# Kernel optimization log

Measured on AMD Instinct MI355X. Metric: run time of the kernel, lower is better.

Reference implementation:

```python
import jax, jax.numpy as jnp
import numpy as np


def setup_inputs() -> dict:
    key = jax.random.key(0)
    k1, k2, k3, k4, k5 = jax.random.split(key, 5)
    b, c, k, h, w = 8, 512, 19, 128, 128
    x = jax.random.normal(k1, (b, c, h, w), dtype=jnp.float32)
    # mask_conv: 1x1 conv ichn->ochn (weight [k, c], bias [k])
    Wm = jax.random.normal(k2, (k, c), dtype=jnp.float32) * (1.0 / np.sqrt(c))
    bm = jax.random.normal(k3, (k,), dtype=jnp.float32) * 0.02
    # filter_conv: grouped 1x1 conv, groups=k -> per-class [c_out, c_in] matmul
    Wf = jax.random.normal(k4, (k, c, c), dtype=jnp.float32) * (1.0 / np.sqrt(c))
    bf = jax.random.normal(k5, (k, c), dtype=jnp.float32) * 0.02
    return {"x": x, "Wm": Wm, "bm": bm, "Wf": Wf, "bf": bf}


def reference(x, Wm, bm, Wf, bf):
    b, c, h, w = x.shape
    k = Wm.shape[0]
    # mask_conv (1x1) + sigmoid -> [b, k, h, w]
    pre_mask = jnp.einsum('bchw,kc->bkhw', x, Wm) + bm[None, :, None, None]
    mask = jax.nn.sigmoid(pre_mask)
    # masked pooling: bmm(mask [b,k,hw], feat [b,hw,c]) / (h*w) -> [b, k, c]
    class_feat = jnp.einsum('bkhw,bchw->bkc', mask, x) / (h * w)
    # grouped 1x1 filter_conv: per class k, [c_out, c_in] GEMM on class_feat
    filters = jnp.einsum('koc,bkc->bko', Wf, class_feat) + bf[None, :, :]  # [b, k, c]
    # per-sample dynamic 1x1 conv (groups=b) == batched GEMM over channels
    pred = jnp.einsum('bkc,bchw->bkhw', filters, x)
    return pred
```

## Files before the change

kernel.cpp:

```cpp
#include <hip/hip_runtime.h>
#include <math.h>

#define BB 8
#define CC 512
#define KK 19
#define HWHW 16384
#define INV_HW (1.0f/16384.0f)

typedef __attribute__((ext_vector_type(8))) short bf16x8;
typedef __attribute__((ext_vector_type(4))) short s16x4;
typedef __attribute__((ext_vector_type(4))) float f32x4;

__device__ __forceinline__ unsigned short f2bf(float f) {
    unsigned int u = __float_as_uint(f);
    u = (u + 0x7fffu + ((u >> 16) & 1u)) >> 16;
    return (unsigned short)u;
}

__global__ __launch_bounds__(256) void k_s1(const float* __restrict__ x,
                                            const float* __restrict__ Wm,
                                            const float* __restrict__ bm,
                                            unsigned short* __restrict__ mask) {
    __shared__ short wm[20 * CC];
    __shared__ short xt[128 * 64];
    const int tid = threadIdx.x;
    const int b = blockIdx.x >> 7;
    const int p0 = (blockIdx.x & 127) << 7;
    const float* xb = x + ((size_t)b * CC) * HWHW + p0;

    for (int u = tid; u < 20 * 128; u += 256) {
        const int k = u >> 7;
        const int c4 = (u & 127) << 2;
        float4 w = {0.f, 0.f, 0.f, 0.f};
        if (k < KK) w = *(const float4*)(Wm + k * CC + c4);
        s16x4 v = { (short)f2bf(w.x), (short)f2bf(w.y), (short)f2bf(w.z), (short)f2bf(w.w) };
        *(s16x4*)&wm[(k << 9) + (((c4 >> 3) ^ (k & 7)) << 3) + (c4 & 7)] = v;
    }

    const int wv = tid >> 6, ln = tid & 63;
    const int lm = ln & 15, q = ln >> 4;
    const f32x4 zz = {0.f, 0.f, 0.f, 0.f};
    f32x4 acc[2][2];
    acc[0][0] = zz; acc[0][1] = zz; acc[1][0] = zz; acc[1][1] = zz;

    for (int cs = 0; cs < 8; ++cs) {
        __syncthreads();
#pragma unroll
        for (int r = 0; r < 2; ++r) {
            const int u = tid + (r << 8);
            const int cg = u >> 5;
            const int p = (u & 31) << 2;
            const float* src = xb + (size_t)((cs << 6) + (cg << 2)) * HWHW + p;
            float4 F0 = *(const float4*)(src);
            float4 F1 = *(const float4*)(src + HWHW);
            float4 F2 = *(const float4*)(src + 2 * HWHW);
            float4 F3 = *(const float4*)(src + 3 * HWHW);
            const float* G0 = (const float*)&F0;
            const float* G1 = (const float*)&F1;
            const float* G2 = (const float*)&F2;
            const float* G3 = (const float*)&F3;
#pragma unroll
            for (int j = 0; j < 4; ++j) {
                const int pr = p + j;
                s16x4 v = { (short)f2bf(G0[j]), (short)f2bf(G1[j]),
                            (short)f2bf(G2[j]), (short)f2bf(G3[j]) };
                *(s16x4*)&xt[(pr << 6) + (((cg >> 1) ^ (pr & 7)) << 3) + ((cg & 1) << 2)] = v;
            }
        }
        __syncthreads();
#pragma unroll
        for (int ks = 0; ks < 2; ++ks) {
            const int gch = (cs << 3) + (ks << 2) + q;
            const int m1 = (lm < 3) ? (16 + lm) : 19;
            bf16x8 a0 = *(const bf16x8*)&wm[(lm << 9) + ((gch ^ (lm & 7)) << 3)];
            bf16x8 a1 = *(const bf16x8*)&wm[(m1 << 9) + ((gch ^ (m1 & 7)) << 3)];
            const int lch = (ks << 2) + q;
#pragma unroll
            for (int nt = 0; nt < 2; ++nt) {
                const int pr = (((wv << 1) + nt) << 4) + lm;
                bf16x8 bf_ = *(const bf16x8*)&xt[(pr << 6) + ((lch ^ (pr & 7)) << 3)];
                acc[0][nt] = __builtin_amdgcn_mfma_f32_16x16x32_bf16(a0, bf_, acc[0][nt], 0, 0, 0);
                acc[1][nt] = __builtin_amdgcn_mfma_f32_16x16x32_bf16(a1, bf_, acc[1][nt], 0, 0, 0);
            }
        }
    }

    unsigned short* mb = mask + ((size_t)b * KK) * HWHW + p0;
#pragma unroll
    for (int mt = 0; mt < 2; ++mt)
#pragma unroll
        for (int r = 0; r < 4; ++r) {
            const int k = (mt << 4) + (q << 2) + r;
            if (k < KK) {
                const float bias = bm[k];
#pragma unroll
                for (int nt = 0; nt < 2; ++nt) {
                    const int p = (((wv << 1) + nt) << 4) + lm;
                    const float t = acc[mt][nt][r] + bias;
                    mb[(size_t)k * HWHW + p] = f2bf(1.0f / (1.0f + __expf(-t)));
                }
            }
        }
}

__global__ __launch_bounds__(256) void k_s2(const float* __restrict__ x,
                                            const unsigned short* __restrict__ mask,
                                            float* __restrict__ cf_part) {
    __shared__ short mt_[20 * 64];
    __shared__ short xtl[64 * 64];
    const int tid = threadIdx.x;
    const int s = blockIdx.x & 15;
    const int ct = (blockIdx.x >> 4) & 7;
    const int b = blockIdx.x >> 7;
    const int wv = tid >> 6, ln = tid & 63;
    const int lm = ln & 15, q = ln >> 4;
    const float* xb = x + ((size_t)b * CC + (ct << 6)) * HWHW + (s << 10);
    const unsigned short* mbs = mask + ((size_t)b * KK) * HWHW + (s << 10);

    const f32x4 zz = {0.f, 0.f, 0.f, 0.f};
    f32x4 acc[2];
    acc[0] = zz; acc[1] = zz;

    for (int kp = 0; kp < 16; ++kp) {
        __syncthreads();
        if (tid < 160) {
            const int k = tid >> 3, ch = tid & 7;
            uint4 v = {0u, 0u, 0u, 0u};
            if (k < KK) v = *(const uint4*)(mbs + (size_t)k * HWHW + (kp << 6) + (ch << 3));
            *(uint4*)&mt_[(k << 6) + ((ch ^ (k & 7)) << 3)] = v;
        }
#pragma unroll
        for (int r = 0; r < 4; ++r) {
            const int u = tid + (r << 8);
            const int c = u >> 4;
            const int pq = u & 15;
            float4 f = *(const float4*)(xb + (size_t)c * HWHW + (kp << 6) + (pq << 2));
            s16x4 v = { (short)f2bf(f.x), (short)f2bf(f.y), (short)f2bf(f.z), (short)f2bf(f.w) };
            *(s16x4*)&xtl[(c << 6) + (((pq >> 1) ^ (c & 7)) << 3) + ((pq & 1) << 2)] = v;
        }
        __syncthreads();
#pragma unroll
        for (int ks = 0; ks < 2; ++ks) {
            const int pch = (ks << 2) + q;
            const int cr = (wv << 4) + lm;
            bf16x8 bf_ = *(const bf16x8*)&xtl[(cr << 6) + ((pch ^ (cr & 7)) << 3)];
            const int m1 = (lm < 3) ? (16 + lm) : 19;
            bf16x8 a0 = *(const bf16x8*)&mt_[(lm << 6) + ((pch ^ (lm & 7)) << 3)];
            bf16x8 a1 = *(const bf16x8*)&mt_[(m1 << 6) + ((pch ^ (m1 & 7)) << 3)];
            acc[0] = __builtin_amdgcn_mfma_f32_16x16x32_bf16(a0, bf_, acc[0], 0, 0, 0);
            acc[1] = __builtin_amdgcn_mfma_f32_16x16x32_bf16(a1, bf_, acc[1], 0, 0, 0);
        }
    }

    float* dst = cf_part + ((size_t)(s * BB + b) * KK) * CC + (ct << 6) + (wv << 4) + lm;
#pragma unroll
    for (int mt = 0; mt < 2; ++mt)
#pragma unroll
        for (int r = 0; r < 4; ++r) {
            const int k = (mt << 4) + (q << 2) + r;
            if (k < KK) dst[(size_t)k * CC] = acc[mt][r];
        }
}

__global__ __launch_bounds__(256) void k_s2r(const float* __restrict__ part,
                                             float* __restrict__ cf) {
    const int i = blockIdx.x * 256 + threadIdx.x;
    if (i >= BB * KK * CC) return;
    const int b = i / (KK * CC);
    const int rem = i - b * (KK * CC);
    float sum = 0.0f;
#pragma unroll
    for (int s = 0; s < 16; ++s)
        sum += part[((size_t)(s * BB + b) * KK) * CC + rem];
    cf[i] = sum * INV_HW;
}

__global__ __launch_bounds__(256) void k_filters(const float* __restrict__ Wf,
                                                 const float* __restrict__ bf,
                                                 const float* __restrict__ cf,
                                                 float* __restrict__ fil) {
    const int blk = blockIdx.x;
    const int k = blk >> 7;
    const int o = ((blk & 127) << 2) + (threadIdx.x >> 6);
    const int lane = threadIdx.x & 63;
    const float* wrow = Wf + ((size_t)k * CC + o) * CC;

    float acc[BB];
#pragma unroll
    for (int b = 0; b < BB; ++b) acc[b] = 0.0f;
#pragma unroll
    for (int j = 0; j < CC / 64; ++j) {
        const int c = lane + (j << 6);
        const float wv = wrow[c];
#pragma unroll
        for (int b = 0; b < BB; ++b)
            acc[b] += wv * cf[((size_t)b * KK + k) * CC + c];
    }
#pragma unroll
    for (int b = 0; b < BB; ++b) {
#pragma unroll
        for (int off = 32; off > 0; off >>= 1)
            acc[b] += __shfl_down(acc[b], off, 64);
    }
    if (lane == 0) {
        const float bias = bf[k * CC + o];
#pragma unroll
        for (int b = 0; b < BB; ++b)
            fil[((size_t)b * KK + k) * CC + o] = acc[b] + bias;
    }
}

__global__ __launch_bounds__(256) void k_s4(const float* __restrict__ x,
                                            const float* __restrict__ fil,
                                            float* __restrict__ out) {
    __shared__ short wm[20 * CC];
    __shared__ short xt[128 * 64];
    const int tid = threadIdx.x;
    const int b = blockIdx.x >> 7;
    const int p0 = (blockIdx.x & 127) << 7;
    const float* xb = x + ((size_t)b * CC) * HWHW + p0;
    const float* fb = fil + ((size_t)b * KK) * CC;

    for (int u = tid; u < 20 * 128; u += 256) {
        const int k = u >> 7;
        const int c4 = (u & 127) << 2;
        float4 w = {0.f, 0.f, 0.f, 0.f};
        if (k < KK) w = *(const float4*)(fb + k * CC + c4);
        s16x4 v = { (short)f2bf(w.x), (short)f2bf(w.y), (short)f2bf(w.z), (short)f2bf(w.w) };
        *(s16x4*)&wm[(k << 9) + (((c4 >> 3) ^ (k & 7)) << 3) + (c4 & 7)] = v;
    }

    const int wv = tid >> 6, ln = tid & 63;
    const int lm = ln & 15, q = ln >> 4;
    const f32x4 zz = {0.f, 0.f, 0.f, 0.f};
    f32x4 acc[2][2];
    acc[0][0] = zz; acc[0][1] = zz; acc[1][0] = zz; acc[1][1] = zz;

    for (int cs = 0; cs < 8; ++cs) {
        __syncthreads();
#pragma unroll
        for (int r = 0; r < 2; ++r) {
            const int u = tid + (r << 8);
            const int cg = u >> 5;
            const int p = (u & 31) << 2;
            const float* src = xb + (size_t)((cs << 6) + (cg << 2)) * HWHW + p;
            float4 F0 = *(const float4*)(src);
            float4 F1 = *(const float4*)(src + HWHW);
            float4 F2 = *(const float4*)(src + 2 * HWHW);
            float4 F3 = *(const float4*)(src + 3 * HWHW);
            const float* G0 = (const float*)&F0;
            const float* G1 = (const float*)&F1;
            const float* G2 = (const float*)&F2;
            const float* G3 = (const float*)&F3;
#pragma unroll
            for (int j = 0; j < 4; ++j) {
                const int pr = p + j;
                s16x4 v = { (short)f2bf(G0[j]), (short)f2bf(G1[j]),
                            (short)f2bf(G2[j]), (short)f2bf(G3[j]) };
                *(s16x4*)&xt[(pr << 6) + (((cg >> 1) ^ (pr & 7)) << 3) + ((cg & 1) << 2)] = v;
            }
        }
        __syncthreads();
#pragma unroll
        for (int ks = 0; ks < 2; ++ks) {
            const int gch = (cs << 3) + (ks << 2) + q;
            const int m1 = (lm < 3) ? (16 + lm) : 19;
            bf16x8 a0 = *(const bf16x8*)&wm[(lm << 9) + ((gch ^ (lm & 7)) << 3)];
            bf16x8 a1 = *(const bf16x8*)&wm[(m1 << 9) + ((gch ^ (m1 & 7)) << 3)];
            const int lch = (ks << 2) + q;
#pragma unroll
            for (int nt = 0; nt < 2; ++nt) {
                const int pr = (((wv << 1) + nt) << 4) + lm;
                bf16x8 bf_ = *(const bf16x8*)&xt[(pr << 6) + ((lch ^ (pr & 7)) << 3)];
                acc[0][nt] = __builtin_amdgcn_mfma_f32_16x16x32_bf16(a0, bf_, acc[0][nt], 0, 0, 0);
                acc[1][nt] = __builtin_amdgcn_mfma_f32_16x16x32_bf16(a1, bf_, acc[1][nt], 0, 0, 0);
            }
        }
    }

    float* ob = out + ((size_t)b * KK) * HWHW + p0;
#pragma unroll
    for (int mt = 0; mt < 2; ++mt)
#pragma unroll
        for (int r = 0; r < 4; ++r) {
            const int k = (mt << 4) + (q << 2) + r;
            if (k < KK) {
#pragma unroll
                for (int nt = 0; nt < 2; ++nt) {
                    const int p = (((wv << 1) + nt) << 4) + lm;
                    ob[(size_t)k * HWHW + p] = acc[mt][nt][r];
                }
            }
        }
}

extern "C" void kernel_launch(void* const* d_in, const int* in_sizes, int n_in,
                              void* d_out, int out_size, void* d_ws, size_t ws_size,
                              hipStream_t stream) {
    const float* x  = (const float*)d_in[0];
    const float* Wm = (const float*)d_in[1];
    const float* bm = (const float*)d_in[2];
    const float* Wf = (const float*)d_in[3];
    const float* bf = (const float*)d_in[4];
    float* out = (float*)d_out;

    unsigned short* mask = (unsigned short*)d_ws;
    float* cf_part = (float*)((char*)d_ws + (size_t)BB * KK * HWHW * 2);
    float* cf  = cf_part + (size_t)16 * BB * KK * CC;
    float* fil = cf + (size_t)BB * KK * CC;

    k_s1<<<1024, 256, 0, stream>>>(x, Wm, bm, mask);
    k_s2<<<1024, 256, 0, stream>>>(x, mask, cf_part);
    k_s2r<<<(BB * KK * CC + 255) / 256, 256, 0, stream>>>(cf_part, cf);
    k_filters<<<KK * 128, 256, 0, stream>>>(Wf, bf, cf, fil);
    k_s4<<<1024, 256, 0, stream>>>(x, fil, out);
}
```

Before: 477.8 us.

## Double-buffer x tiles with register prefetch and single barrier in streaming kernels

The three x-streaming kernels (mask conv, masked pooling, dynamic conv) now prefetch the next channel or pixel chunk of x into registers while the current chunk is converted and stored into one of two LDS buffers. This drops one of the two barriers per iteration. Float-to-bf16 conversion switches to the packed hardware instruction, and occupancy hints are added to launch bounds. The aim is to hide global-load latency behind MFMA work, at the cost of higher register and LDS use, which may limit occupancy.

After: 470.3 us. No clear change (-1.6%).

```diff
diff --git a/kernel.cpp b/kernel.cpp
--- a/kernel.cpp
+++ b/kernel.cpp
@@ -17,12 +17,18 @@
     return (unsigned short)u;
 }
 
-__global__ __launch_bounds__(256) void k_s1(const float* __restrict__ x,
-                                            const float* __restrict__ Wm,
-                                            const float* __restrict__ bm,
-                                            unsigned short* __restrict__ mask) {
+__device__ __forceinline__ unsigned int pk_bf16(float a, float b) {
+    unsigned int r;
+    asm("v_cvt_pk_bf16_f32 %0, %1, %2" : "=v"(r) : "v"(a), "v"(b));
+    return r;
+}
+
+__global__ __launch_bounds__(256, 3) void k_s1(const float* __restrict__ x,
+                                               const float* __restrict__ Wm,
+                                               const float* __restrict__ bm,
+                                               unsigned short* __restrict__ mask) {
     __shared__ short wm[20 * CC];
-    __shared__ short xt[128 * 64];
+    __shared__ short xt[2][128 * 64];
     const int tid = threadIdx.x;
     const int b = blockIdx.x >> 7;
     const int p0 = (blockIdx.x & 127) << 7;
@@ -43,31 +49,48 @@
     f32x4 acc[2][2];
     acc[0][0] = zz; acc[0][1] = zz; acc[1][0] = zz; acc[1][1] = zz;
 
+    const int cg0 = tid >> 5;
+    const int pA  = (tid & 31) << 2;
+    const float* sA = xb + (size_t)(cg0 << 2) * HWHW + pA;
+    const float* sB = xb + (size_t)((cg0 + 8) << 2) * HWHW + pA;
+
+    float4 Fa[8], Fb[8];
+#pragma unroll
+    for (int j = 0; j < 4; ++j) {
+        Fa[j]     = *(const float4*)(sA + (size_t)j * HWHW);
+        Fa[4 + j] = *(const float4*)(sB + (size_t)j * HWHW);
+    }
+
+#pragma unroll
     for (int cs = 0; cs < 8; ++cs) {
-        __syncthreads();
-#pragma unroll
-        for (int r = 0; r < 2; ++r) {
-            const int u = tid + (r << 8);
-            const int cg = u >> 5;
-            const int p = (u & 31) << 2;
-            const float* src = xb + (size_t)((cs << 6) + (cg << 2)) * HWHW + p;
-            float4 F0 = *(const float4*)(src);
-            float4 F1 = *(const float4*)(src + HWHW);
-            float4 F2 = *(const float4*)(src + 2 * HWHW);
-            float4 F3 = *(const float4*)(src + 3 * HWHW);
-            const float* G0 = (const float*)&F0;
-            const float* G1 = (const float*)&F1;
-            const float* G2 = (const float*)&F2;
-            const float* G3 = (const float*)&F3;
+        const float4* cur = (cs & 1) ? Fb : Fa;
+        float4* nxt = (cs & 1) ? Fa : Fb;
+        if (cs < 7) {
+            const size_t co = (size_t)((cs + 1) << 6) * HWHW;
 #pragma unroll
             for (int j = 0; j < 4; ++j) {
-                const int pr = p + j;
-                s16x4 v = { (short)f2bf(G0[j]), (short)f2bf(G1[j]),
-                            (short)f2bf(G2[j]), (short)f2bf(G3[j]) };
-                *(s16x4*)&xt[(pr << 6) + (((cg >> 1) ^ (pr & 7)) << 3) + ((cg & 1) << 2)] = v;
-            }
-        }
-        __syncthreads();
+                nxt[j]     = *(const float4*)(sA + co + (size_t)j * HWHW);
+                nxt[4 + j] = *(const float4*)(sB + co + (size_t)j * HWHW);
+            }
+        }
+        short* xts = (short*)xt[cs & 1];
+#pragma unroll
+        for (int h = 0; h < 2; ++h) {
+            const int cg = cg0 + (h << 3);
+            const float* G0 = (const float*)&cur[(h << 2) + 0];
+            const float* G1 = (const float*)&cur[(h << 2) + 1];
+            const float* G2 = (const float*)&cur[(h << 2) + 2];
+            const float* G3 = (const float*)&cur[(h << 2) + 3];
+#pragma unroll
+            for (int j = 0; j < 4; ++j) {
+                const int pr = pA + j;
+                uint2 v = make_uint2(pk_bf16(G0[j], G1[j]), pk_bf16(G2[j], G3[j]));
+                *(uint2*)&xts[(pr << 6) + (((cg >> 1) ^ (pr & 7)) << 3) + ((cg & 1) << 2)] = v;
+            }
+        }
+        asm volatile("s_waitcnt lgkmcnt(0)" ::: "memory");
+        __builtin_amdgcn_s_barrier();
+        asm volatile("" ::: "memory");
 #pragma unroll
         for (int ks = 0; ks < 2; ++ks) {
             const int gch = (cs << 3) + (ks << 2) + q;
@@ -78,9 +101,9 @@
 #pragma unroll
             for (int nt = 0; nt < 2; ++nt) {
                 const int pr = (((wv << 1) + nt) << 4) + lm;
-                bf16x8 bf_ = *(const bf16x8*)&xt[(pr << 6) + ((lch ^ (pr & 7)) << 3)];
-                acc[0][nt] = __builtin_amdgcn_mfma_f32_16x16x32_bf16(a0, bf_, acc[0][nt], 0, 0, 0);
-                acc[1][nt] = __builtin_amdgcn_mfma_f32_16x16x32_bf16(a1, bf_, acc[1][nt], 0, 0, 0);
+                bf16x8 bv = *(const bf16x8*)&xts[(pr << 6) + ((lch ^ (pr & 7)) << 3)];
+                acc[0][nt] = __builtin_amdgcn_mfma_f32_16x16x32_bf16(a0, bv, acc[0][nt], 0, 0, 0);
+                acc[1][nt] = __builtin_amdgcn_mfma_f32_16x16x32_bf16(a1, bv, acc[1][nt], 0, 0, 0);
             }
         }
     }
@@ -103,11 +126,11 @@
         }
 }
 
-__global__ __launch_bounds__(256) void k_s2(const float* __restrict__ x,
-                                            const unsigned short* __restrict__ mask,
-                                            float* __restrict__ cf_part) {
-    __shared__ short mt_[20 * 64];
-    __shared__ short xtl[64 * 64];
+__global__ __launch_bounds__(256, 4) void k_s2(const float* __restrict__ x,
+                                               const unsigned short* __restrict__ mask,
+                                               float* __restrict__ cf_part) {
+    __shared__ short mt_[2][20 * 64];
+    __shared__ short xtl[2][64 * 64];
     const int tid = threadIdx.x;
     const int s = blockIdx.x & 15;
     const int ct = (blockIdx.x >> 4) & 7;
@@ -117,38 +140,59 @@
     const float* xb = x + ((size_t)b * CC + (ct << 6)) * HWHW + (s << 10);
     const unsigned short* mbs = mask + ((size_t)b * KK) * HWHW + (s << 10);
 
+    const int mk = tid >> 3, mch = tid & 7;
+    const int xc = tid >> 4;
+    const int pq = tid & 15;
+
     const f32x4 zz = {0.f, 0.f, 0.f, 0.f};
     f32x4 acc[2];
     acc[0] = zz; acc[1] = zz;
 
+    float4 Xa[4], Xb[4];
+    uint4 Ma = make_uint4(0u,0u,0u,0u), Mb = make_uint4(0u,0u,0u,0u);
+
+    if (tid < 160 && mk < KK) Ma = *(const uint4*)(mbs + (size_t)mk * HWHW + (mch << 3));
+#pragma unroll
+    for (int r = 0; r < 4; ++r)
+        Xa[r] = *(const float4*)(xb + (size_t)(xc + (r << 4)) * HWHW + (pq << 2));
+
+#pragma unroll
     for (int kp = 0; kp < 16; ++kp) {
-        __syncthreads();
-        if (tid < 160) {
-            const int k = tid >> 3, ch = tid & 7;
-            uint4 v = {0u, 0u, 0u, 0u};
-            if (k < KK) v = *(const uint4*)(mbs + (size_t)k * HWHW + (kp << 6) + (ch << 3));
-            *(uint4*)&mt_[(k << 6) + ((ch ^ (k & 7)) << 3)] = v;
-        }
+        const float4* curX = (kp & 1) ? Xb : Xa;
+        float4* nxtX = (kp & 1) ? Xa : Xb;
+        const uint4 curM = (kp & 1) ? Mb : Ma;
+        uint4* nxtM = (kp & 1) ? &Ma : &Mb;
+        if (kp < 15) {
+            if (tid < 160 && mk < KK)
+                *nxtM = *(const uint4*)(mbs + (size_t)mk * HWHW + ((kp + 1) << 6) + (mch << 3));
+#pragma unroll
+            for (int r = 0; r < 4; ++r)
+                nxtX[r] = *(const float4*)(xb + (size_t)(xc + (r << 4)) * HWHW + ((kp + 1) << 6) + (pq << 2));
+        }
+        short* mts = (short*)mt_[kp & 1];
+        short* xls = (short*)xtl[kp & 1];
+        if (tid < 160)
+            *(uint4*)&mts[(mk << 6) + ((mch ^ (mk & 7)) << 3)] = curM;
 #pragma unroll
         for (int r = 0; r < 4; ++r) {
-            const int u = tid + (r << 8);
-            const int c = u >> 4;
-            const int pq = u & 15;
-            float4 f = *(const float4*)(xb + (size_t)c * HWHW + (kp << 6) + (pq << 2));
-            s16x4 v = { (short)f2bf(f.x), (short)f2bf(f.y), (short)f2bf(f.z), (short)f2bf(f.w) };
-            *(s16x4*)&xtl[(c << 6) + (((pq >> 1) ^ (c & 7)) << 3) + ((pq & 1) << 2)] = v;
-        }
-        __syncthreads();
+            const int c = xc + (r << 4);
+            const float* G = (const float*)&curX[r];
+            uint2 v = make_uint2(pk_bf16(G[0], G[1]), pk_bf16(G[2], G[3]));
+            *(uint2*)&xls[(c << 6) + (((pq >> 1) ^ (c & 7)) << 3) + ((pq & 1) << 2)] = v;
+        }
+        asm volatile("s_waitcnt lgkmcnt(0)" ::: "memory");
+        __builtin_amdgcn_s_barrier();
+        asm volatile("" ::: "memory");
 #pragma unroll
         for (int ks = 0; ks < 2; ++ks) {
             const int pch = (ks << 2) + q;
             const int cr = (wv << 4) + lm;
-            bf16x8 bf_ = *(const bf16x8*)&xtl[(cr << 6) + ((pch ^ (cr & 7)) << 3)];
+            bf16x8 bv = *(const bf16x8*)&xls[(cr << 6) + ((pch ^ (cr & 7)) << 3)];
             const int m1 = (lm < 3) ? (16 + lm) : 19;
-            bf16x8 a0 = *(const bf16x8*)&mt_[(lm << 6) + ((pch ^ (lm & 7)) << 3)];
-            bf16x8 a1 = *(const bf16x8*)&mt_[(m1 << 6) + ((pch ^ (m1 & 7)) << 3)];
-            acc[0] = __builtin_amdgcn_mfma_f32_16x16x32_bf16(a0, bf_, acc[0], 0, 0, 0);
-            acc[1] = __builtin_amdgcn_mfma_f32_16x16x32_bf16(a1, bf_, acc[1], 0, 0, 0);
+            bf16x8 a0 = *(const bf16x8*)&mts[(lm << 6) + ((pch ^ (lm & 7)) << 3)];
+            bf16x8 a1 = *(const bf16x8*)&mts[(m1 << 6) + ((pch ^ (m1 & 7)) << 3)];
+            acc[0] = __builtin_amdgcn_mfma_f32_16x16x32_bf16(a0, bv, acc[0], 0, 0, 0);
+            acc[1] = __builtin_amdgcn_mfma_f32_16x16x32_bf16(a1, bv, acc[1], 0, 0, 0);
         }
     }
 
@@ -210,11 +254,11 @@
     }
 }
 
-__global__ __launch_bounds__(256) void k_s4(const float* __restrict__ x,
-                                            const float* __restrict__ fil,
-                                            float* __restrict__ out) {
+__global__ __launch_bounds__(256, 3) void k_s4(const float* __restrict__ x,
+                                               const float* __restrict__ fil,
+                                               float* __restrict__ out) {
     __shared__ short wm[20 * CC];
-    __shared__ short xt[128 * 64];
+    __shared__ short xt[2][128 * 64];
     const int tid = threadIdx.x;
     const int b = blockIdx.x >> 7;
     const int p0 = (blockIdx.x & 127) << 7;
@@ -236,31 +280,48 @@
     f32x4 acc[2][2];
     acc[0][0] = zz; acc[0][1] = zz; acc[1][0] = zz; acc[1][1] = zz;
 
+    const int cg0 = tid >> 5;
+    const int pA  = (tid & 31) << 2;
+    const float* sA = xb + (size_t)(cg0 << 2) * HWHW + pA;
+    const float* sB = xb + (size_t)((cg0 + 8) << 2) * HWHW + pA;
+
+    float4 Fa[8], Fb[8];
+#pragma unroll
+    for (int j = 0; j < 4; ++j) {
+        Fa[j]     = *(const float4*)(sA + (size_t)j * HWHW);
+        Fa[4 + j] = *(const float4*)(sB + (size_t)j * HWHW);
+    }
+
+#pragma unroll
     for (int cs = 0; cs < 8; ++cs) {
-        __syncthreads();
-#pragma unroll
-        for (int r = 0; r < 2; ++r) {
-            const int u = tid + (r << 8);
-            const int cg = u >> 5;
-            const int p = (u & 31) << 2;
-            const float* src = xb + (size_t)((cs << 6) + (cg << 2)) * HWHW + p;
-            float4 F0 = *(const float4*)(src);
-            float4 F1 = *(const float4*)(src + HWHW);
-            float4 F2 = *(const float4*)(src + 2 * HWHW);
-            float4 F3 = *(const float4*)(src + 3 * HWHW);
-            const float* G0 = (const float*)&F0;
-            const float* G1 = (const float*)&F1;
-            const float* G2 = (const float*)&F2;
-            const float* G3 = (const float*)&F3;
+        const float4* cur = (cs & 1) ? Fb : Fa;
+        float4* nxt = (cs & 1) ? Fa : Fb;
+        if (cs < 7) {
+            const size_t co = (size_t)((cs + 1) << 6) * HWHW;
 #pragma unroll
             for (int j = 0; j < 4; ++j) {
-                const int pr = p + j;
-                s16x4 v = { (short)f2bf(G0[j]), (short)f2bf(G1[j]),
-                            (short)f2bf(G2[j]), (short)f2bf(G3[j]) };
-                *(s16x4*)&xt[(pr << 6) + (((cg >> 1) ^ (pr & 7)) << 3) + ((cg & 1) << 2)] = v;
-            }
-        }
-        __syncthreads();
+                nxt[j]     = *(const float4*)(sA + co + (size_t)j * HWHW);
+                nxt[4 + j] = *(const float4*)(sB + co + (size_t)j * HWHW);
+            }
+        }
+        short* xts = (short*)xt[cs & 1];
+#pragma unroll
+        for (int h = 0; h < 2; ++h) {
+            const int cg = cg0 + (h << 3);
+            const float* G0 = (const float*)&cur[(h << 2) + 0];
+            const float* G1 = (const float*)&cur[(h << 2) + 1];
+            const float* G2 = (const float*)&cur[(h << 2) + 2];
+            const float* G3 = (const float*)&cur[(h << 2) + 3];
+#pragma unroll
+            for (int j = 0; j < 4; ++j) {
+                const int pr = pA + j;
+                uint2 v = make_uint2(pk_bf16(G0[j], G1[j]), pk_bf16(G2[j], G3[j]));
+                *(uint2*)&xts[(pr << 6) + (((cg >> 1) ^ (pr & 7)) << 3) + ((cg & 1) << 2)] = v;
+            }
+        }
+        asm volatile("s_waitcnt lgkmcnt(0)" ::: "memory");
+        __builtin_amdgcn_s_barrier();
+        asm volatile("" ::: "memory");
 #pragma unroll
         for (int ks = 0; ks < 2; ++ks) {
             const int gch = (cs << 3) + (ks << 2) + q;
@@ -271,9 +332,9 @@
 #pragma unroll
             for (int nt = 0; nt < 2; ++nt) {
                 const int pr = (((wv << 1) + nt) << 4) + lm;
-                bf16x8 bf_ = *(const bf16x8*)&xt[(pr << 6) + ((lch ^ (pr & 7)) << 3)];
-                acc[0][nt] = __builtin_amdgcn_mfma_f32_16x16x32_bf16(a0, bf_, acc[0][nt], 0, 0, 0);
-                acc[1][nt] = __builtin_amdgcn_mfma_f32_16x16x32_bf16(a1, bf_, acc[1][nt], 0, 0, 0);
+                bf16x8 bv = *(const bf16x8*)&xts[(pr << 6) + ((lch ^ (pr & 7)) << 3)];
+                acc[0][nt] = __builtin_amdgcn_mfma_f32_16x16x32_bf16(a0, bv, acc[0][nt], 0, 0, 0);
+                acc[1][nt] = __builtin_amdgcn_mfma_f32_16x16x32_bf16(a1, bv, acc[1][nt], 0, 0, 0);
             }
         }
     }
```
